# Kernel tuning notes

Measured on AMD Instinct MI355X. Metric: run time of the kernel, lower is better.

The kernel has to match this reference:

```python
import jax, jax.numpy as jnp
import numpy as np
import math

B, S, HID = 2, 2048, 1152
NH, NKV = 16, 4
HD = HID // NH  # 72
GROUPS = NH // NKV  # 4
ROPE_BASE = 10000.0


def setup_inputs() -> dict:
    key = jax.random.key(0)
    ks = jax.random.split(key, 5)
    hidden_states = jax.random.normal(ks[0], (B, S, HID), dtype=jnp.float32)
    # causal additive mask: 0 on/below diagonal, -1e9 above
    causal = jnp.tril(jnp.ones((S, S), dtype=jnp.bool_))
    attention_mask = jnp.where(causal, 0.0, -1e9).astype(jnp.float32)[None, None]
    scale = 0.02
    wq = jax.random.normal(ks[1], (HID, HID), dtype=jnp.float32) * scale
    wk = jax.random.normal(ks[2], (NKV * HD, HID), dtype=jnp.float32) * scale
    wv = jax.random.normal(ks[3], (NKV * HD, HID), dtype=jnp.float32) * scale
    wo = jax.random.normal(ks[4], (HID, HID), dtype=jnp.float32) * scale
    return {"hidden_states": hidden_states, "attention_mask": attention_mask,
            "wq": wq, "wk": wk, "wv": wv, "wo": wo}


def _rotate_half(x):
    x1, x2 = jnp.split(x, 2, axis=-1)
    return jnp.concatenate((-x2, x1), axis=-1)


def _rope_cos_sin(seq_len, dim, dtype):
    inv_freq = 1.0 / (ROPE_BASE ** (jnp.arange(0, dim, 2, dtype=jnp.float32) / dim))
    t = jnp.arange(seq_len, dtype=jnp.float32)
    freqs = jnp.outer(t, inv_freq)          # [S, dim/2]
    emb = jnp.concatenate((freqs, freqs), axis=-1)  # [S, dim]
    return jnp.cos(emb).astype(dtype), jnp.sin(emb).astype(dtype)


def reference(hidden_states, attention_mask, wq, wk, wv, wo):
    b, s, _ = hidden_states.shape
    # projections (nn.Linear: x @ W.T)
    q = (hidden_states @ wq.T).reshape(b, s, NH, HD).transpose(0, 2, 1, 3)    # [b,nh,s,hd]
    k = (hidden_states @ wk.T).reshape(b, s, NKV, HD).transpose(0, 2, 1, 3)   # [b,nkv,s,hd]
    v = (hidden_states @ wv.T).reshape(b, s, NKV, HD).transpose(0, 2, 1, 3)
    # RoPE
    cos, sin = _rope_cos_sin(s, HD, hidden_states.dtype)
    cos, sin = cos[None, None], sin[None, None]  # [1,1,s,hd]
    q = q * cos + _rotate_half(q) * sin
    k = k * cos + _rotate_half(k) * sin
    # expand kv heads (repeat_interleave over head dim)
    k = jnp.repeat(k, GROUPS, axis=1)  # [b,nh,s,hd]
    v = jnp.repeat(v, GROUPS, axis=1)
    scores = jnp.einsum('bhqd,bhkd->bhqk', q, k) / math.sqrt(HD)
    scores = scores + attention_mask
    attn = jax.nn.softmax(scores.astype(jnp.float32), axis=-1).astype(q.dtype)
    out = jnp.einsum('bhqk,bhkd->bhqd', attn, v)
    out = out.transpose(0, 2, 1, 3).reshape(b, s, HID)
    return out @ wo.T
```

## Files before the change

kernel.cpp:

```cpp
#include <hip/hip_runtime.h>
#include <hip/hip_bf16.h>
#include <cstddef>

#define B_   2
#define S_   2048
#define HID_ 1152
#define NH_  16
#define NKV_ 4
#define HD_  72
#define MTOT (B_ * S_)
#define KVDIM (NKV_ * HD_)

typedef float f32x4 __attribute__((ext_vector_type(4)));
typedef short bf16x8 __attribute__((ext_vector_type(8)));
typedef short s4v __attribute__((ext_vector_type(4)));

__device__ __forceinline__ float bf2f(short x) {
  unsigned int u = ((unsigned int)(unsigned short)x) << 16;
  return __builtin_bit_cast(float, u);
}
__device__ __forceinline__ short f2bf(float f) {
  unsigned int u = __builtin_bit_cast(unsigned int, f);
  u += 0x7fff + ((u >> 16) & 1);
  return (short)(u >> 16);
}

__device__ __forceinline__ float fast_exp2(float x) {
#if __has_builtin(__builtin_amdgcn_exp2f)
  return __builtin_amdgcn_exp2f(x);
#else
  return exp2f(x);
#endif
}

__device__ __forceinline__ void async16(const short* g, short* lds) {
  __builtin_amdgcn_global_load_lds((const __attribute__((address_space(1))) void*)g,
                                   (__attribute__((address_space(3))) void*)lds,
                                   16, 0, 0);
}

__global__ void k_cvt_all(const float4* __restrict__ s0, const float4* __restrict__ s1,
                          const float4* __restrict__ s2, const float4* __restrict__ s3,
                          const float4* __restrict__ s4,
                          s4v* __restrict__ d0, s4v* __restrict__ d1, s4v* __restrict__ d2,
                          s4v* __restrict__ d3, s4v* __restrict__ d4,
                          float2* __restrict__ tab,
                          int n0, int n1, int n2, int n3, int n4t) {
  int ncvt = n0 + n1 + n2 + n3 + n4t;
  int total = ncvt + S_ * 36;
  for (int i = blockIdx.x * blockDim.x + threadIdx.x; i < total;
       i += gridDim.x * blockDim.x) {
    if (i < ncvt) {
      const float4* s;
      s4v* d;
      int off = i;
      if (off < n0) { s = s0; d = d0; }
      else {
        off -= n0;
        if (off < n1) { s = s1; d = d1; }
        else {
          off -= n1;
          if (off < n2) { s = s2; d = d2; }
          else {
            off -= n2;
            if (off < n3) { s = s3; d = d3; }
            else { off -= n3; s = s4; d = d4; }
          }
        }
      }
      float4 v = s[off];
      s4v o = { f2bf(v.x), f2bf(v.y), f2bf(v.z), f2bf(v.w) };
      d[off] = o;
    } else {
      int idx = i - ncvt;
      int ii = idx % 36, s = idx / 36;
      float freq = powf(10000.0f, -(float)ii / 36.0f);
      float a = (float)s * freq;
      tab[idx] = make_float2(cosf(a), sinf(a));
    }
  }
}

__global__ void k_post(short* __restrict__ Qb, short* __restrict__ Kb,
                       const short* __restrict__ Vb, short* __restrict__ Vt,
                       const float2* __restrict__ tab) {
  int idx = blockIdx.x * blockDim.x + threadIdx.x;
  const int nrope = MTOT * 20 * 36;
  if (idx < nrope) {
    int i = idx % 36;
    int t = idx / 36;
    int hh = t % 20;
    int m = t / 20;
    int s = m & (S_ - 1);
    float2 cs = tab[s * 36 + i];
    short* p = (hh < 16) ? Qb + (size_t)m * HID_ + hh * HD_
                         : Kb + (size_t)m * KVDIM + (hh - 16) * HD_;
    float x1 = bf2f(p[i]), x2 = bf2f(p[i + 36]);
    p[i]      = f2bf(x1 * cs.x - x2 * cs.y);
    p[i + 36] = f2bf(x2 * cs.x + x1 * cs.y);
  } else {
    idx -= nrope;
    if (idx >= 8 * 80 * S_) return;
    int s = idx & (S_ - 1);
    int t2 = idx >> 11;
    int d = t2 % 80;
    int bkv = t2 / 80;
    int b = bkv >> 2, kv = bkv & 3;
    short v = 0;
    if (d < HD_) v = Vb[((size_t)(b * S_ + s)) * KVDIM + kv * HD_ + d];
    else if (d == HD_) v = (short)0x3F80;
    Vt[idx] = v;
  }
}

#define BM 128
#define BN 128
#define BK 32

__global__ __launch_bounds__(256) void k_gemm_qkv(const short* __restrict__ A,
                                                  const short* __restrict__ Wq,
                                                  const short* __restrict__ Wk,
                                                  const short* __restrict__ Wv,
                                                  short* __restrict__ Qo,
                                                  short* __restrict__ Ko,
                                                  short* __restrict__ Vo) {
  const int K = HID_, NTOT = 1728;
  __shared__ short As[BM * BK];
  __shared__ short Bs[BN * BK];
  const int tid = threadIdx.x;
  const int l = tid & 63;
  const int w = tid >> 6;
  const int bm = blockIdx.x * BM;
  const int bn = blockIdx.y * BN;
  const int wr = (w >> 1) * 64;
  const int wc = (w & 1) * 64;
  const int c15 = l & 15, g = l >> 4;
  const int r0 = tid >> 2;
  const int c0 = (tid & 3) * 8;

  f32x4 acc[4][4] = {};

  for (int k0 = 0; k0 < K; k0 += BK) {
#pragma unroll
    for (int it = 0; it < 2; ++it) {
      int ar = bm + it * 64 + r0;
      int br = bn + it * 64 + r0;
      if (br > NTOT - 1) br = NTOT - 1;
      const short* bsrc;
      if (br < 1152)      bsrc = Wq + (size_t)br * K;
      else if (br < 1440) bsrc = Wk + (size_t)(br - 1152) * K;
      else                bsrc = Wv + (size_t)(br - 1440) * K;
      async16(A + (size_t)ar * K + k0 + c0, &As[(it * 64 + r0) * BK + c0]);
      async16(bsrc + k0 + c0, &Bs[(it * 64 + r0) * BK + c0]);
    }
    __syncthreads();
    bf16x8 af[4], bfr[4];
#pragma unroll
    for (int t = 0; t < 4; ++t) {
      af[t]  = *(const bf16x8*)&As[(wr + t * 16 + c15) * BK + g * 8];
      bfr[t] = *(const bf16x8*)&Bs[(wc + t * 16 + c15) * BK + g * 8];
    }
#pragma unroll
    for (int mt = 0; mt < 4; ++mt)
#pragma unroll
      for (int nt = 0; nt < 4; ++nt)
        acc[mt][nt] = __builtin_amdgcn_mfma_f32_16x16x32_bf16(af[mt], bfr[nt], acc[mt][nt], 0, 0, 0);
    __syncthreads();
  }

#pragma unroll
  for (int mt = 0; mt < 4; ++mt)
#pragma unroll
    for (int nt = 0; nt < 4; ++nt)
#pragma unroll
      for (int j = 0; j < 4; ++j) {
        int row = bm + wr + mt * 16 + g * 4 + j;
        int col = bn + wc + nt * 16 + c15;
        short val = f2bf(acc[mt][nt][j]);
        if (col < 1152)      Qo[(size_t)row * HID_ + col] = val;
        else if (col < 1440) Ko[(size_t)row * KVDIM + col - 1152] = val;
        else if (col < NTOT) Vo[(size_t)row * KVDIM + col - 1440] = val;
      }
}

__global__ __launch_bounds__(256) void k_gemm_o(const short* __restrict__ A,
                                                const short* __restrict__ Bm,
                                                float* __restrict__ C,
                                                int M, int N, int K) {
  __shared__ short As[BM * BK];
  __shared__ short Bs[BN * BK];
  const int tid = threadIdx.x;
  const int l = tid & 63;
  const int w = tid >> 6;
  const int bm = blockIdx.x * BM;
  const int bn = blockIdx.y * BN;
  const int wr = (w >> 1) * 64;
  const int wc = (w & 1) * 64;
  const int c15 = l & 15, g = l >> 4;
  const int r0 = tid >> 2;
  const int c0 = (tid & 3) * 8;

  f32x4 acc[4][4] = {};

  for (int k0 = 0; k0 < K; k0 += BK) {
#pragma unroll
    for (int it = 0; it < 2; ++it) {
      int ar = bm + it * 64 + r0;
      int br = bn + it * 64 + r0;
      if (br > N - 1) br = N - 1;
      async16(A + (size_t)ar * K + k0 + c0, &As[(it * 64 + r0) * BK + c0]);
      async16(Bm + (size_t)br * K + k0 + c0, &Bs[(it * 64 + r0) * BK + c0]);
    }
    __syncthreads();
    bf16x8 af[4], bfr[4];
#pragma unroll
    for (int t = 0; t < 4; ++t) {
      af[t]  = *(const bf16x8*)&As[(wr + t * 16 + c15) * BK + g * 8];
      bfr[t] = *(const bf16x8*)&Bs[(wc + t * 16 + c15) * BK + g * 8];
    }
#pragma unroll
    for (int mt = 0; mt < 4; ++mt)
#pragma unroll
      for (int nt = 0; nt < 4; ++nt)
        acc[mt][nt] = __builtin_amdgcn_mfma_f32_16x16x32_bf16(af[mt], bfr[nt], acc[mt][nt], 0, 0, 0);
    __syncthreads();
  }

#pragma unroll
  for (int mt = 0; mt < 4; ++mt)
#pragma unroll
    for (int nt = 0; nt < 4; ++nt)
#pragma unroll
      for (int j = 0; j < 4; ++j) {
        int row = bm + wr + mt * 16 + g * 4 + j;
        int col = bn + wc + nt * 16 + c15;
        if (col < N) C[(size_t)row * N + col] = acc[mt][nt][j];
      }
}

#define QB 16
#define KT 64

__global__ __launch_bounds__(256, 2) void k_flash(const short* __restrict__ Q,
                                                  const short* __restrict__ Kg,
                                                  const short* __restrict__ Vt,
                                                  short* __restrict__ O) {
  const int bid = blockIdx.x;
  const int bkv = bid & 7;
  const int qt = 127 - (bid >> 3);
  const int b = bkv >> 2, kv = bkv & 3;
  const int tid = threadIdx.x;
  const int w = tid >> 6, l = tid & 63;
  const int h = kv * 4 + w;
  const int q0 = qt * QB;
  const int c15 = l & 15, g = l >> 4;

  __shared__ short lds[24064];
  short* Ks0 = lds;
  short* Vs0 = lds + 4608;
  short* Ks1 = lds + 9728;
  short* Vs1 = lds + 14336;
  short* Ps  = lds + 19456 + w * 1152;

  const float SCL = 0.117851130f * 1.4426950408889634f;
  const float SHIFT = 8.0f;

  const short* Qbase = Q + (size_t)(b * S_) * HID_ + h * HD_;
  const short* Kbase = Kg + (size_t)(b * S_) * KVDIM + kv * HD_;
  const short* Vbase = Vt + (size_t)bkv * 80 * S_;

  bf16x8 qf[3];
  const bf16x8 zfrag = {0, 0, 0, 0, 0, 0, 0, 0};
  {
    int row = q0 + c15;
#pragma unroll
    for (int ks = 0; ks < 3; ++ks) {
      int d0 = ks * 32 + g * 8;
      qf[ks] = (d0 < HD_) ? *(const bf16x8*)(Qbase + (size_t)row * HID_ + d0) : zfrag;
    }
#pragma unroll
    for (int ks = 0; ks < 3; ++ks)
#pragma unroll
      for (int e = 0; e < 8; ++e)
        qf[ks][e] = f2bf(bf2f(qf[ks][e]) * SCL);
  }

  f32x4 accO[5] = {};

  const int nkt = (q0 + QB + KT - 1) / KT;
  const int nfull = (QB * qt + 1) >> 6;

  auto STAGE = [&](int kb, short* Kd, short* Vd) {
    const short* kp = Kbase + (size_t)kb * KVDIM;
    const short* vp = Vbase + kb;
#pragma unroll
    for (int i = 0; i < 5; ++i) {
      int c = tid + 256 * i;
      if (c < 576) {
        int row = c / 9, cc = c - row * 9;
        async16(kp + (size_t)row * KVDIM + cc * 8, &Kd[c * 8]);
      } else if (c < 1216) {
        int c2 = c - 576;
        int row = c2 >> 3, slot = c2 & 7;
        async16(vp + (size_t)row * S_ + ((slot ^ (row & 7)) << 3), &Vd[c2 * 8]);
      }
    }
  };

  STAGE(0, Ks0, Vs0);
  short *Ksc = Ks0, *Vsc = Vs0, *Ksn = Ks1, *Vsn = Vs1;

  for (int kt = 0; kt < nkt; ++kt) {
    asm volatile("s_waitcnt vmcnt(0)" ::: "memory");
    __builtin_amdgcn_sched_barrier(0);
    __syncthreads();
    if (kt + 1 < nkt) STAGE((kt + 1) * KT, Ksn, Vsn);

    const int kbase = kt * KT;

    f32x4 sc[4] = {};
    __builtin_amdgcn_s_setprio(1);
#pragma unroll
    for (int ct = 0; ct < 4; ++ct)
#pragma unroll
      for (int ks = 0; ks < 3; ++ks) {
        bf16x8 kf = *(const bf16x8*)&Ksc[(ct * 16 + c15) * 72 + ks * 32 + g * 8];
        sc[ct] = __builtin_amdgcn_mfma_f32_16x16x32_bf16(qf[ks], kf, sc[ct], 0, 0, 0);
      }
    __builtin_amdgcn_s_setprio(0);

    const int qrow = q0 + g * 4;
    if (kt >= nfull) {
#pragma unroll
      for (int ct = 0; ct < 4; ++ct) {
        int col = kbase + ct * 16 + c15;
#pragma unroll
        for (int j = 0; j < 4; ++j)
          if (col > qrow + j) sc[ct][j] = -1e30f;
      }
    }
#pragma unroll
    for (int ct = 0; ct < 4; ++ct)
#pragma unroll
      for (int j = 0; j < 4; ++j)
        sc[ct][j] = fast_exp2(sc[ct][j] - SHIFT);

#pragma unroll
    for (int ct = 0; ct < 4; ++ct)
#pragma unroll
      for (int j = 0; j < 4; ++j)
        Ps[(g * 4 + j) * 72 + ct * 16 + c15] = f2bf(sc[ct][j]);
    asm volatile("s_waitcnt lgkmcnt(0)" ::: "memory");
    __builtin_amdgcn_sched_barrier(0);
    bf16x8 pa0 = *(const bf16x8*)&Ps[c15 * 72 + g * 8];
    bf16x8 pa1 = *(const bf16x8*)&Ps[c15 * 72 + 32 + g * 8];

    __builtin_amdgcn_s_setprio(1);
#pragma unroll
    for (int dt = 0; dt < 5; ++dt) {
      int vrow = dt * 16 + c15;
      bf16x8 vb0 = *(const bf16x8*)&Vsc[vrow * 64 + (((0 * 4 + g) ^ (vrow & 7)) << 3)];
      bf16x8 vb1 = *(const bf16x8*)&Vsc[vrow * 64 + (((1 * 4 + g) ^ (vrow & 7)) << 3)];
      accO[dt] = __builtin_amdgcn_mfma_f32_16x16x32_bf16(pa0, vb0, accO[dt], 0, 0, 0);
      accO[dt] = __builtin_amdgcn_mfma_f32_16x16x32_bf16(pa1, vb1, accO[dt], 0, 0, 0);
    }
    __builtin_amdgcn_s_setprio(0);

    short* t1 = Ksc; Ksc = Ksn; Ksn = t1;
    short* t2 = Vsc; Vsc = Vsn; Vsn = t2;
  }

  float lj[4];
#pragma unroll
  for (int j = 0; j < 4; ++j)
    lj[j] = 1.0f / __shfl(accO[4][j], (l & 48) | 8);
#pragma unroll
  for (int dt = 0; dt < 5; ++dt) {
    int d = dt * 16 + c15;
    if (d < HD_) {
#pragma unroll
      for (int j = 0; j < 4; ++j) {
        int row = q0 + g * 4 + j;
        O[(size_t)(b * S_ + row) * HID_ + h * HD_ + d] = f2bf(accO[dt][j] * lj[j]);
      }
    }
  }
}

extern "C" void kernel_launch(void* const* d_in, const int* in_sizes, int n_in,
                              void* d_out, int out_size, void* d_ws, size_t ws_size,
                              hipStream_t stream) {
  const float* hs = (const float*)d_in[0];
  const float* wq = (const float*)d_in[2];
  const float* wk = (const float*)d_in[3];
  const float* wv = (const float*)d_in[4];
  const float* wo = (const float*)d_in[5];

  char* ws = (char*)d_ws;
  short* Xb  = (short*)(ws + 0);
  short* Qb  = (short*)(ws + 9437184);
  short* Kb  = (short*)(ws + 18874368);
  short* Vb  = (short*)(ws + 21233664);
  short* Vt  = (short*)(ws + 23592960);
  short* Ob  = (short*)(ws + 26214400);
  short* wqb = (short*)(ws + 35651584);
  short* wkb = (short*)(ws + 38305792);
  short* wvb = (short*)(ws + 38969344);
  short* wob = (short*)(ws + 39632896);
  float2* tab = (float2*)(ws + 42287104);

  k_cvt_all<<<2048, 256, 0, stream>>>(
      (const float4*)hs, (const float4*)wq, (const float4*)wk, (const float4*)wv,
      (const float4*)wo,
      (s4v*)Xb, (s4v*)wqb, (s4v*)wkb, (s4v*)wvb, (s4v*)wob, tab,
      MTOT * HID_ / 4, HID_ * HID_ / 4, KVDIM * HID_ / 4, KVDIM * HID_ / 4,
      HID_ * HID_ / 4);

  k_gemm_qkv<<<dim3(32, 14), 256, 0, stream>>>(Xb, wqb, wkb, wvb, Qb, Kb, Vb);

  {
    int total = MTOT * 20 * 36 + 8 * 80 * S_;
    k_post<<<(total + 255) / 256, 256, 0, stream>>>(Qb, Kb, Vb, Vt, tab);
  }

  k_flash<<<1024, 256, 0, stream>>>(Qb, Kb, Vt, Ob);

  k_gemm_o<<<dim3(32, 9), 256, 0, stream>>>(Ob, wob, (float*)d_out, MTOT, HID_, HID_);
}
```

Baseline: 131.8 us.

## Fuse RoPE into QKV GEMM epilogue via interleaved weight-row permutation

Rows of the Q and K weights are permuted during the bf16 conversion so that each rotate-half pair (i, i+36) lands in adjacent output columns. The QKV GEMM epilogue then applies RoPE in registers, using a lane shuffle to fetch the partner value and the cos/sin table. This removes the separate read-modify-write pass over Q and K, which survives only as a V-transpose kernel. Q and K are now stored in the same permuted head-dimension order, so attention dot products stay unchanged. The cost is per-element table loads and shuffles in the GEMM epilogue.

```diff
diff --git a/kernel.cpp b/kernel.cpp
--- a/kernel.cpp
+++ b/kernel.cpp
@@ -54,13 +54,14 @@
       const float4* s;
       s4v* d;
       int off = i;
+      bool perm = false;
       if (off < n0) { s = s0; d = d0; }
       else {
         off -= n0;
-        if (off < n1) { s = s1; d = d1; }
+        if (off < n1) { s = s1; d = d1; perm = true; }
         else {
           off -= n1;
-          if (off < n2) { s = s2; d = d2; }
+          if (off < n2) { s = s2; d = d2; perm = true; }
           else {
             off -= n2;
             if (off < n3) { s = s3; d = d3; }
@@ -70,7 +71,14 @@
       }
       float4 v = s[off];
       s4v o = { f2bf(v.x), f2bf(v.y), f2bf(v.z), f2bf(v.w) };
-      d[off] = o;
+      int out = off;
+      if (perm) {
+        int r = off / 288, k4 = off - r * 288;
+        int h = r / 72, ii = r - h * 72;
+        int pr = h * 72 + (ii < 36 ? 2 * ii : 2 * (ii - 36) + 1);
+        out = pr * 288 + k4;
+      }
+      d[out] = o;
     } else {
       int idx = i - ncvt;
       int ii = idx % 36, s = idx / 36;
@@ -81,36 +89,18 @@
   }
 }
 
-__global__ void k_post(short* __restrict__ Qb, short* __restrict__ Kb,
-                       const short* __restrict__ Vb, short* __restrict__ Vt,
-                       const float2* __restrict__ tab) {
+__global__ void k_vt(const short* __restrict__ Vb, short* __restrict__ Vt) {
   int idx = blockIdx.x * blockDim.x + threadIdx.x;
-  const int nrope = MTOT * 20 * 36;
-  if (idx < nrope) {
-    int i = idx % 36;
-    int t = idx / 36;
-    int hh = t % 20;
-    int m = t / 20;
-    int s = m & (S_ - 1);
-    float2 cs = tab[s * 36 + i];
-    short* p = (hh < 16) ? Qb + (size_t)m * HID_ + hh * HD_
-                         : Kb + (size_t)m * KVDIM + (hh - 16) * HD_;
-    float x1 = bf2f(p[i]), x2 = bf2f(p[i + 36]);
-    p[i]      = f2bf(x1 * cs.x - x2 * cs.y);
-    p[i + 36] = f2bf(x2 * cs.x + x1 * cs.y);
-  } else {
-    idx -= nrope;
-    if (idx >= 8 * 80 * S_) return;
-    int s = idx & (S_ - 1);
-    int t2 = idx >> 11;
-    int d = t2 % 80;
-    int bkv = t2 / 80;
-    int b = bkv >> 2, kv = bkv & 3;
-    short v = 0;
-    if (d < HD_) v = Vb[((size_t)(b * S_ + s)) * KVDIM + kv * HD_ + d];
-    else if (d == HD_) v = (short)0x3F80;
-    Vt[idx] = v;
-  }
+  if (idx >= 8 * 80 * S_) return;
+  int s = idx & (S_ - 1);
+  int t2 = idx >> 11;
+  int d = t2 % 80;
+  int bkv = t2 / 80;
+  int b = bkv >> 2, kv = bkv & 3;
+  short v = 0;
+  if (d < HD_) v = Vb[((size_t)(b * S_ + s)) * KVDIM + kv * HD_ + d];
+  else if (d == HD_) v = (short)0x3F80;
+  Vt[idx] = v;
 }
 
 #define BM 128
@@ -123,7 +113,8 @@
                                                   const short* __restrict__ Wv,
                                                   short* __restrict__ Qo,
                                                   short* __restrict__ Ko,
-                                                  short* __restrict__ Vo) {
+                                                  short* __restrict__ Vo,
+                                                  const float2* __restrict__ tab) {
   const int K = HID_, NTOT = 1728;
   __shared__ short As[BM * BK];
   __shared__ short Bs[BN * BK];
@@ -171,16 +162,25 @@
 #pragma unroll
   for (int mt = 0; mt < 4; ++mt)
 #pragma unroll
-    for (int nt = 0; nt < 4; ++nt)
+    for (int nt = 0; nt < 4; ++nt) {
+      int col = bn + wc + nt * 16 + c15;
+      int ch = col < 1152 ? col : col - 1152;
+      int ii = (ch % 72) >> 1;
+      bool isqk = col < 1440;
 #pragma unroll
       for (int j = 0; j < 4; ++j) {
         int row = bm + wr + mt * 16 + g * 4 + j;
-        int col = bn + wc + nt * 16 + c15;
-        short val = f2bf(acc[mt][nt][j]);
+        float v = acc[mt][nt][j];
+        float p = __shfl_xor(v, 1);
+        float2 cs = tab[(row & (S_ - 1)) * 36 + ii];
+        float r = (c15 & 1) ? (v * cs.x + p * cs.y)
+                            : (v * cs.x - p * cs.y);
+        short val = f2bf(isqk ? r : v);
         if (col < 1152)      Qo[(size_t)row * HID_ + col] = val;
         else if (col < 1440) Ko[(size_t)row * KVDIM + col - 1152] = val;
         else if (col < NTOT) Vo[(size_t)row * KVDIM + col - 1440] = val;
       }
+    }
 }
 
 __global__ __launch_bounds__(256) void k_gemm_o(const short* __restrict__ A,
@@ -416,12 +416,9 @@
       MTOT * HID_ / 4, HID_ * HID_ / 4, KVDIM * HID_ / 4, KVDIM * HID_ / 4,
       HID_ * HID_ / 4);
 
-  k_gemm_qkv<<<dim3(32, 14), 256, 0, stream>>>(Xb, wqb, wkb, wvb, Qb, Kb, Vb);
-
-  {
-    int total = MTOT * 20 * 36 + 8 * 80 * S_;
-    k_post<<<(total + 255) / 256, 256, 0, stream>>>(Qb, Kb, Vb, Vt, tab);
-  }
+  k_gemm_qkv<<<dim3(32, 14), 256, 0, stream>>>(Xb, wqb, wkb, wvb, Qb, Kb, Vb, tab);
+
+  k_vt<<<(8 * 80 * S_ + 255) / 256, 256, 0, stream>>>(Vb, Vt);
 
   k_flash<<<1024, 256, 0, stream>>>(Qb, Kb, Vt, Ob);
 
```

New measurement: 135.0 us. 2.4% more time.
